# Performance work log

Measured on AMD Instinct MI355X. Metric: run time of the kernel, lower is better.

## Reference

```python
import jax, jax.numpy as jnp
import numpy as np

B, S, D = 2, 1024, 1024
H, KV, HD = 16, 4, 64
E, F = 8, 3584
EPS = 1e-5
TOP_K = 2


def setup_inputs() -> dict:
    key = jax.random.key(0)
    ks = jax.random.split(key, 12)
    sc = 0.02
    inv_freq = 1.0 / (10000.0 ** (np.arange(0, HD, 2, dtype=np.float32) / HD))
    freqs = np.outer(np.arange(S, dtype=np.float32), inv_freq)
    emb = np.concatenate([freqs, freqs], axis=-1)  # [S, HD]
    return {
        'x': jax.random.normal(ks[0], (B, S, D), jnp.float32),
        'ln1_w': jnp.ones((D,), jnp.float32),
        'ln2_w': jnp.ones((D,), jnp.float32),
        'wq': jax.random.normal(ks[1], (H * HD, D), jnp.float32) * sc,
        'wk': jax.random.normal(ks[2], (KV * HD, D), jnp.float32) * sc,
        'wv': jax.random.normal(ks[3], (KV * HD, D), jnp.float32) * sc,
        'wo': jax.random.normal(ks[4], (D, H * HD), jnp.float32) * sc,
        'gate_w': jax.random.normal(ks[5], (E, D), jnp.float32) * sc,
        'w1': jax.random.normal(ks[6], (E, F, D), jnp.float32) * sc,
        'w2': jax.random.normal(ks[7], (E, D, F), jnp.float32) * sc,
        'w3': jax.random.normal(ks[8], (E, F, D), jnp.float32) * sc,
        'cos': jnp.asarray(np.cos(emb)),
        'sin': jnp.asarray(np.sin(emb)),
    }


def _rms_norm(x, w):
    var = jnp.mean(jnp.square(x), axis=-1, keepdims=True)
    return x * jax.lax.rsqrt(var + EPS) * w


def _rotate_half(x):
    x1, x2 = jnp.split(x, 2, axis=-1)
    return jnp.concatenate([-x2, x1], axis=-1)


def _attn(h, wq, wk, wv, wo, cos, sin):
    # h: [B,S,D]
    q = (h @ wq.T).reshape(B, S, H, HD).transpose(0, 2, 1, 3)      # [B,H,S,HD]
    k = (h @ wk.T).reshape(B, S, KV, HD).transpose(0, 2, 1, 3)     # [B,KV,S,HD]
    v = (h @ wv.T).reshape(B, S, KV, HD).transpose(0, 2, 1, 3)
    c = cos[None, None, :S, :]
    s = sin[None, None, :S, :]
    q = q * c + _rotate_half(q) * s
    k = k * c + _rotate_half(k) * s
    k = jnp.repeat(k, H // KV, axis=1)  # GQA expand -> [B,H,S,HD]
    v = jnp.repeat(v, H // KV, axis=1)
    scores = jnp.einsum('bhqd,bhkd->bhqk', q, k) / jnp.sqrt(jnp.float32(HD))
    causal = jnp.tril(jnp.ones((S, S), bool))
    scores = jnp.where(causal[None, None], scores, jnp.float32(-1e30))
    probs = jax.nn.softmax(scores, axis=-1)
    out = jnp.einsum('bhqk,bhkd->bhqd', probs, v)
    out = out.transpose(0, 2, 1, 3).reshape(B, S, H * HD)
    return out @ wo.T


def _moe(h, gate_w, w1, w2, w3):
    T = B * S
    hs = h.reshape(T, D)
    probs = jax.nn.softmax(hs @ gate_w.T, axis=-1)       # [T,E]
    _, sel = jax.lax.top_k(probs, TOP_K)                  # [T,2]
    rw = jnp.take_along_axis(probs, sel, axis=-1)
    rw = rw / jnp.sum(rw, axis=-1, keepdims=True)
    cw = jnp.zeros((T, E), hs.dtype).at[jnp.arange(T)[:, None], sel].add(rw)  # [T,E] combine weights
    h1 = jnp.einsum('td,efd->tef', hs, w1)               # [T,E,F]
    h3 = jnp.einsum('td,efd->tef', hs, w3)
    inter = jax.nn.silu(h1) * h3
    out = jnp.einsum('tef,edf,te->td', inter, w2, cw)
    return out.reshape(B, S, D)


def reference(x, ln1_w, ln2_w, wq, wk, wv, wo, gate_w, w1, w2, w3, cos, sin):
    h = x + _attn(_rms_norm(x, ln1_w), wq, wk, wv, wo, cos, sin)
    h = h + _moe(_rms_norm(h, ln2_w), gate_w, w1, w2, w3)
    return h
```

## Files before the change

### kernel.cpp

```cpp
#include <hip/hip_runtime.h>

typedef unsigned short u16;
using short8 = __attribute__((ext_vector_type(8))) short;
using f32x4  = __attribute__((ext_vector_type(4))) float;

#define TQ   2048
#define DM   1024
#define SLEN 1024
#define FDIM 3584
#define NEXP 8

static __device__ __forceinline__ u16 f2bf(float f) {
  union { float f; unsigned u; } a; a.f = f;
  unsigned r = a.u + 0x7fffu + ((a.u >> 16) & 1u);
  return (u16)(r >> 16);
}
static __device__ __forceinline__ float bf2f(u16 u) {
  union { unsigned u; float f; } a; a.u = ((unsigned)u) << 16;
  return a.f;
}
static __device__ __forceinline__ unsigned cvtpk(float lo, float hi) {
  unsigned r;
  asm volatile("v_cvt_pk_bf16_f32 %0, %1, %2" : "=v"(r) : "v"(lo), "v"(hi));
  return r;
}

static __device__ __forceinline__ void gload16(const void* g, void* l) {
  __builtin_amdgcn_global_load_lds((const __attribute__((address_space(1))) void*)g,
                                   (__attribute__((address_space(3))) void*)l, 16, 0, 0);
}

static __device__ __forceinline__ int swz64(int bid) {
  return (bid & ~63) | ((bid & 7) << 3) | ((bid >> 3) & 7);
}

static __device__ __forceinline__ short8 ldW(const float* base, int row, int g) {
  const float* rp = base + row * 32;
  int x0 = (((g << 1) ^ (row & 7)) << 2);
  int x1 = ((((g << 1) | 1) ^ (row & 7)) << 2);
  float4 f0 = *(const float4*)(rp + x0);
  float4 f1 = *(const float4*)(rp + x1);
  union { uint4 u; short8 s; } c;
  c.u.x = cvtpk(f0.x, f0.y); c.u.y = cvtpk(f0.z, f0.w);
  c.u.z = cvtpk(f1.x, f1.y); c.u.w = cvtpk(f1.z, f1.w);
  return c.s;
}

__global__ __launch_bounds__(256) void rmsnorm_kernel(
    const float* __restrict__ x, const float* __restrict__ w,
    u16* __restrict__ oh, u16* __restrict__ ol, float* __restrict__ of) {
  int t = blockIdx.x, tid = threadIdx.x;
  const float4* xr = (const float4*)(x + (size_t)t * DM);
  float4 v = xr[tid];
  float ss = v.x * v.x + v.y * v.y + v.z * v.z + v.w * v.w;
#pragma unroll
  for (int m = 1; m < 64; m <<= 1) ss += __shfl_xor(ss, m);
  __shared__ float red[4];
  if ((tid & 63) == 0) red[tid >> 6] = ss;
  __syncthreads();
  float tot = red[0] + red[1] + red[2] + red[3];
  float sc = rsqrtf(tot * (1.0f / DM) + 1e-5f);
  float4 wv = ((const float4*)w)[tid];
  float o0 = v.x * sc * wv.x, o1 = v.y * sc * wv.y, o2 = v.z * sc * wv.z, o3 = v.w * sc * wv.w;
  ushort4 hh;
  hh.x = f2bf(o0); hh.y = f2bf(o1); hh.z = f2bf(o2); hh.w = f2bf(o3);
  *(ushort4*)(oh + (size_t)t * DM + tid * 4) = hh;
  if (ol) {
    ushort4 ll;
    ll.x = f2bf(o0 - bf2f(hh.x)); ll.y = f2bf(o1 - bf2f(hh.y));
    ll.z = f2bf(o2 - bf2f(hh.z)); ll.w = f2bf(o3 - bf2f(hh.w));
    *(ushort4*)(ol + (size_t)t * DM + tid * 4) = ll;
  }
  if (of) {
    float4 o4; o4.x = o0; o4.y = o1; o4.z = o2; o4.w = o3;
    ((float4*)(of + (size_t)t * DM))[tid] = o4;
  }
}

__global__ __launch_bounds__(256) void wconv_split_kernel(
    const float* __restrict__ wq, const float* __restrict__ wk,
    const float* __restrict__ wv, const float* __restrict__ wo,
    u16* __restrict__ qkvh, u16* __restrict__ qkvl,
    u16* __restrict__ woh, u16* __restrict__ wol) {
  for (int i = blockIdx.x * 256 + threadIdx.x; i < 655360; i += 640 * 256) {
    int el = i * 4;
    const float* src; u16 *dh, *dl;
    if (el < 1572864) {
      int r = el >> 10, c = el & 1023;
      if (r < 1024) src = wq + el;
      else if (r < 1280) src = wk + (r - 1024) * 1024 + c;
      else src = wv + (r - 1280) * 1024 + c;
      dh = qkvh + el; dl = qkvl + el;
    } else {
      int e2 = el - 1572864;
      src = wo + e2; dh = woh + e2; dl = wol + e2;
    }
    float4 v = *(const float4*)src;
    ushort4 h, l;
    h.x = f2bf(v.x); h.y = f2bf(v.y); h.z = f2bf(v.z); h.w = f2bf(v.w);
    l.x = f2bf(v.x - bf2f(h.x)); l.y = f2bf(v.y - bf2f(h.y));
    l.z = f2bf(v.z - bf2f(h.z)); l.w = f2bf(v.w - bf2f(h.w));
    *(ushort4*)dh = h; *(ushort4*)dl = l;
  }
}

template <bool RESID>
__global__ __launch_bounds__(256) void gemm_split2_kernel(
    const u16* __restrict__ Ah, const u16* __restrict__ Al,
    const u16* __restrict__ Wh, const u16* __restrict__ Wl,
    float* __restrict__ C, const float* __restrict__ resid, int N) {
  __shared__ u16 sAh[2][128][32], sAl[2][128][32], sWh[2][64][32], sWl[2][64][32];
  int lid = swz64(blockIdx.x);
  int bm = lid & 15, bn = lid >> 4;
  int tid = threadIdx.x, lane = tid & 63, w = tid >> 6;
  int wm = w >> 1, wn = w & 1;
  int qi = lane & 15, g = lane >> 4;
  int lr = lane >> 2, lc = (lane & 3) * 8;
  const u16* pa0 = Ah + (size_t)(bm * 128 + w * 16 + lr) * DM + lc;
  const u16* pa1 = pa0 + 64 * DM;
  const u16* pl0 = Al + (size_t)(bm * 128 + w * 16 + lr) * DM + lc;
  const u16* pl1 = pl0 + 64 * DM;
  const u16* pw  = Wh + (size_t)(bn * 64 + w * 16 + lr) * DM + lc;
  const u16* pwl = Wl + (size_t)(bn * 64 + w * 16 + lr) * DM + lc;
  f32x4 acc[4][2] = {};
#define STG2(buf, kk) do { \
    gload16(pa0 + (kk), &sAh[buf][w * 16][0]); \
    gload16(pa1 + (kk), &sAh[buf][64 + w * 16][0]); \
    gload16(pl0 + (kk), &sAl[buf][w * 16][0]); \
    gload16(pl1 + (kk), &sAl[buf][64 + w * 16][0]); \
    gload16(pw  + (kk), &sWh[buf][w * 16][0]); \
    gload16(pwl + (kk), &sWl[buf][w * 16][0]); } while (0)
  STG2(0, 0);
  asm volatile("s_waitcnt vmcnt(0)" ::: "memory");
  __syncthreads();
  for (int ks = 0; ks < 32; ks++) {
    int cur = ks & 1;
    if (ks < 31) STG2(cur ^ 1, (ks + 1) * 32);
    short8 afh[4], afl[4], bfh[2], bfl[2];
#pragma unroll
    for (int i = 0; i < 4; i++) {
      afh[i] = *(short8*)&sAh[cur][wm * 64 + i * 16 + qi][g * 8];
      afl[i] = *(short8*)&sAl[cur][wm * 64 + i * 16 + qi][g * 8];
    }
#pragma unroll
    for (int i = 0; i < 2; i++) {
      bfh[i] = *(short8*)&sWh[cur][wn * 32 + i * 16 + qi][g * 8];
      bfl[i] = *(short8*)&sWl[cur][wn * 32 + i * 16 + qi][g * 8];
    }
#pragma unroll
    for (int mi = 0; mi < 4; mi++)
#pragma unroll
      for (int ni = 0; ni < 2; ni++) {
        f32x4 a = acc[mi][ni];
        a = __builtin_amdgcn_mfma_f32_16x16x32_bf16(afh[mi], bfh[ni], a, 0, 0, 0);
        a = __builtin_amdgcn_mfma_f32_16x16x32_bf16(afl[mi], bfh[ni], a, 0, 0, 0);
        a = __builtin_amdgcn_mfma_f32_16x16x32_bf16(afh[mi], bfl[ni], a, 0, 0, 0);
        acc[mi][ni] = a;
      }
    asm volatile("s_waitcnt vmcnt(0)" ::: "memory");
    __syncthreads();
  }
#undef STG2
#pragma unroll
  for (int mi = 0; mi < 4; mi++)
#pragma unroll
    for (int ni = 0; ni < 2; ni++) {
      int col = bn * 64 + wn * 32 + ni * 16 + qi;
#pragma unroll
      for (int r = 0; r < 4; r++) {
        int row = bm * 128 + wm * 64 + mi * 16 + g * 4 + r;
        float val = acc[mi][ni][r];
        if (RESID) val += resid[(size_t)row * N + col];
        C[(size_t)row * N + col] = val;
      }
    }
}

__global__ __launch_bounds__(256) void rope_split_kernel(
    const float* __restrict__ qkvf,
    const float* __restrict__ cosT, const float* __restrict__ sinT,
    u16* __restrict__ qh, u16* __restrict__ ql, u16* __restrict__ kh, u16* __restrict__ kl,
    u16* __restrict__ vh, u16* __restrict__ vl) {
  int t = blockIdx.x, tid = threadIdx.x;
  int s = t & (SLEN - 1);
  const float* rowp = qkvf + (size_t)t * 1536;
#pragma unroll
  for (int it = 0; it < 2; it++) {
    int i = it * 256 + tid;
    int hh = i >> 5, d = i & 31;
    float c = cosT[s * 64 + d], sn = sinT[s * 64 + d];
    size_t dst = (size_t)t * DM + hh * 64 + d;
    float x1 = rowp[hh * 64 + d], x2 = rowp[hh * 64 + d + 32];
    float o1 = x1 * c - x2 * sn;
    float o2 = x2 * c + x1 * sn;
    u16 h1 = f2bf(o1), h2 = f2bf(o2);
    qh[dst] = h1; qh[dst + 32] = h2;
    ql[dst] = f2bf(o1 - bf2f(h1)); ql[dst + 32] = f2bf(o2 - bf2f(h2));
  }
  if (tid < 128) {
    int hh = tid >> 5, d = tid & 31;
    float c = cosT[s * 64 + d], sn = sinT[s * 64 + d];
    size_t dst = (size_t)t * 256 + hh * 64 + d;
    float x1 = rowp[1024 + hh * 64 + d], x2 = rowp[1024 + hh * 64 + d + 32];
    float o1 = x1 * c - x2 * sn;
    float o2 = x2 * c + x1 * sn;
    u16 h1 = f2bf(o1), h2 = f2bf(o2);
    kh[dst] = h1; kh[dst + 32] = h2;
    kl[dst] = f2bf(o1 - bf2f(h1)); kl[dst + 32] = f2bf(o2 - bf2f(h2));
  }
  {
    size_t dst = (size_t)t * 256 + tid;
    float v = rowp[1280 + tid];
    u16 h = f2bf(v);
    vh[dst] = h; vl[dst] = f2bf(v - bf2f(h));
  }
}

__global__ __launch_bounds__(256) void attn_kernel(
    const u16* __restrict__ qh, const u16* __restrict__ ql,
    const u16* __restrict__ kh, const u16* __restrict__ kl,
    const u16* __restrict__ vh, const u16* __restrict__ vl,
    u16* __restrict__ oh, u16* __restrict__ ol) {
  __shared__ u16 sKh[64][72], sKl[64][72];
  __shared__ u16 sVh[64][72], sVl[64][72];
  __shared__ u16 sPh[4][16][72], sPl[4][16][72];
  int qt = blockIdx.x & 15;
  int bh = blockIdx.x >> 4;
  int b = bh >> 4, h = bh & 15, kvh = h >> 2;
  int tid = threadIdx.x, lane = tid & 63, w = tid >> 6;
  int qi = lane & 15, g = lane >> 4;
  int qrow = qt * 64 + w * 16 + qi;
  size_t qbase = ((size_t)(b * SLEN + qrow)) * DM + h * 64;
  short8 qfh[2], qfl[2];
#pragma unroll
  for (int ds = 0; ds < 2; ds++) {
    qfh[ds] = *(const short8*)(qh + qbase + ds * 32 + g * 8);
    qfl[ds] = *(const short8*)(ql + qbase + ds * 32 + g * 8);
  }
  f32x4 oacc[4] = {};
  float mrun = -1e30f, lrun = 0.f;
  int ktiles = qt + 1;
  for (int kt = 0; kt < ktiles; kt++) {
    __syncthreads();
    {
      int r = tid >> 3, cs = (tid & 7) * 8;
#pragma unroll
      for (int rr = 0; rr < 64; rr += 32) {
        int key = kt * 64 + rr + r;
        size_t src = ((size_t)(b * SLEN + key)) * 256 + kvh * 64 + cs;
        *(short8*)&sKh[rr + r][cs] = *(const short8*)(kh + src);
        *(short8*)&sKl[rr + r][cs] = *(const short8*)(kl + src);
        short8 vv = *(const short8*)(vh + src);
        short8 vv2 = *(const short8*)(vl + src);
#pragma unroll
        for (int j = 0; j < 8; j++) {
          sVh[cs + j][rr + r] = (u16)vv[j];
          sVl[cs + j][rr + r] = (u16)vv2[j];
        }
      }
    }
    __syncthreads();
    f32x4 sa[4];
#pragma unroll
    for (int kf = 0; kf < 4; kf++) {
      f32x4 a = {};
#pragma unroll
      for (int ds = 0; ds < 2; ds++) {
        short8 kfh = *(short8*)&sKh[kf * 16 + qi][ds * 32 + g * 8];
        short8 kfl = *(short8*)&sKl[kf * 16 + qi][ds * 32 + g * 8];
        a = __builtin_amdgcn_mfma_f32_16x16x32_bf16(kfh, qfh[ds], a, 0, 0, 0);
        a = __builtin_amdgcn_mfma_f32_16x16x32_bf16(kfl, qfh[ds], a, 0, 0, 0);
        a = __builtin_amdgcn_mfma_f32_16x16x32_bf16(kfh, qfl[ds], a, 0, 0, 0);
      }
      sa[kf] = a;
    }
    int qg = qt * 64 + w * 16 + qi;
    float sv[4][4];
    float tmax = -1e30f;
#pragma unroll
    for (int kf = 0; kf < 4; kf++)
#pragma unroll
      for (int r = 0; r < 4; r++) {
        int key = kt * 64 + kf * 16 + g * 4 + r;
        float s = sa[kf][r] * 0.125f;
        s = (key <= qg) ? s : -1e30f;
        sv[kf][r] = s;
        tmax = fmaxf(tmax, s);
      }
    tmax = fmaxf(tmax, __shfl_xor(tmax, 16));
    tmax = fmaxf(tmax, __shfl_xor(tmax, 32));
    float mn = fmaxf(mrun, tmax);
    float alpha = expf(mrun - mn);
    float psum = 0.f;
#pragma unroll
    for (int kf = 0; kf < 4; kf++) {
      float p0 = expf(sv[kf][0] - mn), p1 = expf(sv[kf][1] - mn);
      float p2 = expf(sv[kf][2] - mn), p3 = expf(sv[kf][3] - mn);
      psum += p0 + p1 + p2 + p3;
      ushort4 ph, pl;
      ph.x = f2bf(p0); ph.y = f2bf(p1); ph.z = f2bf(p2); ph.w = f2bf(p3);
      pl.x = f2bf(p0 - bf2f(ph.x)); pl.y = f2bf(p1 - bf2f(ph.y));
      pl.z = f2bf(p2 - bf2f(ph.z)); pl.w = f2bf(p3 - bf2f(ph.w));
      *(ushort4*)&sPh[w][qi][kf * 16 + g * 4] = ph;
      *(ushort4*)&sPl[w][qi][kf * 16 + g * 4] = pl;
    }
    psum += __shfl_xor(psum, 16);
    psum += __shfl_xor(psum, 32);
    lrun = lrun * alpha + psum;
    mrun = mn;
#pragma unroll
    for (int df = 0; df < 4; df++) {
      oacc[df][0] *= alpha; oacc[df][1] *= alpha;
      oacc[df][2] *= alpha; oacc[df][3] *= alpha;
    }
#pragma unroll
    for (int ks = 0; ks < 2; ks++) {
      short8 pfh = *(short8*)&sPh[w][qi][ks * 32 + g * 8];
      short8 pfl = *(short8*)&sPl[w][qi][ks * 32 + g * 8];
#pragma unroll
      for (int df = 0; df < 4; df++) {
        short8 vfh = *(short8*)&sVh[df * 16 + qi][ks * 32 + g * 8];
        short8 vfl = *(short8*)&sVl[df * 16 + qi][ks * 32 + g * 8];
        f32x4 a = oacc[df];
        a = __builtin_amdgcn_mfma_f32_16x16x32_bf16(vfh, pfh, a, 0, 0, 0);
        a = __builtin_amdgcn_mfma_f32_16x16x32_bf16(vfl, pfh, a, 0, 0, 0);
        a = __builtin_amdgcn_mfma_f32_16x16x32_bf16(vfh, pfl, a, 0, 0, 0);
        oacc[df] = a;
      }
    }
  }
  float inv = 1.0f / lrun;
  size_t obase = ((size_t)(b * SLEN + qt * 64 + w * 16 + qi)) * DM + h * 64;
#pragma unroll
  for (int df = 0; df < 4; df++) {
    float o0 = oacc[df][0] * inv, o1 = oacc[df][1] * inv;
    float o2 = oacc[df][2] * inv, o3 = oacc[df][3] * inv;
    ushort4 hh, ll;
    hh.x = f2bf(o0); hh.y = f2bf(o1); hh.z = f2bf(o2); hh.w = f2bf(o3);
    ll.x = f2bf(o0 - bf2f(hh.x)); ll.y = f2bf(o1 - bf2f(hh.y));
    ll.z = f2bf(o2 - bf2f(hh.z)); ll.w = f2bf(o3 - bf2f(hh.w));
    *(ushort4*)(oh + obase + df * 16 + g * 4) = hh;
    *(ushort4*)(ol + obase + df * 16 + g * 4) = ll;
  }
}

__global__ void zero8_kernel(int* p) { if (threadIdx.x < 8) p[threadIdx.x] = 0; }

__global__ __launch_bounds__(64) void gate_kernel(
    const float* __restrict__ hf, const float* __restrict__ gw,
    int* cnt, int* tok_e, int* tok_pos, float* tok_w) {
  int t = blockIdx.x, lane = threadIdx.x;
  float acc[8] = {0, 0, 0, 0, 0, 0, 0, 0};
  for (int i = lane; i < DM; i += 64) {
    float h = hf[(size_t)t * DM + i];
#pragma unroll
    for (int e = 0; e < 8; e++) acc[e] += h * gw[e * DM + i];
  }
#pragma unroll
  for (int e = 0; e < 8; e++)
#pragma unroll
    for (int m = 1; m < 64; m <<= 1) acc[e] += __shfl_xor(acc[e], m);
  if (lane == 0) {
    int i0 = 0;
#pragma unroll
    for (int e = 1; e < 8; e++) if (acc[e] > acc[i0]) i0 = e;
    int i1 = -1;
#pragma unroll
    for (int e = 0; e < 8; e++) if (e != i0 && (i1 < 0 || acc[e] > acc[i1])) i1 = e;
    float w0 = 1.0f;
    float w1 = expf(acc[i1] - acc[i0]);
    float rs = 1.0f / (w0 + w1);
    int p0 = atomicAdd(&cnt[i0], 1);
    int p1 = atomicAdd(&cnt[i1], 1);
    tok_e[t * 2] = i0; tok_e[t * 2 + 1] = i1;
    tok_pos[t * 2] = p0; tok_pos[t * 2 + 1] = p1;
    tok_w[t * 2] = w0 * rs; tok_w[t * 2 + 1] = w1 * rs;
  }
}

__global__ void schedule_kernel(const int* cnt, int* offs, int* mt,
                                int* row_e, int* row_bm) {
  if (threadIdx.x == 0) {
    int s = 0, m = 0;
    for (int e = 0; e < 8; e++) {
      offs[e] = s;
      int nb = (cnt[e] + 127) >> 7;
      for (int i = 0; i < nb; i++) { row_e[m] = e; row_bm[m] = i; m++; }
      s += cnt[e];
    }
    *mt = m;
  }
}

__global__ __launch_bounds__(256) void gather_kernel(
    const u16* __restrict__ hn2b, const int* __restrict__ tok_e,
    const int* __restrict__ tok_pos, const float* __restrict__ tok_w,
    const int* __restrict__ offs, u16* __restrict__ Xg,
    int* __restrict__ pair_tok, int* __restrict__ pair_slot, float* __restrict__ pair_w) {
  int t = blockIdx.x;
#pragma unroll
  for (int slot = 0; slot < 2; slot++) {
    int e = tok_e[t * 2 + slot];
    int p = offs[e] + tok_pos[t * 2 + slot];
    ((ushort4*)(Xg + (size_t)p * DM))[threadIdx.x] =
        ((const ushort4*)(hn2b + (size_t)t * DM))[threadIdx.x];
    if (threadIdx.x == 0) {
      pair_tok[p] = t; pair_slot[p] = slot; pair_w[p] = tok_w[t * 2 + slot];
    }
  }
}

__global__ __launch_bounds__(256) void moe_gemm13_kernel(
    const u16* __restrict__ Xg, const float* __restrict__ w1,
    const float* __restrict__ w3, const int* __restrict__ cnt,
    const int* __restrict__ offs, const int* __restrict__ mt,
    const int* __restrict__ row_e, const int* __restrict__ row_bm,
    u16* __restrict__ inter) {
  __shared__ u16 sA[3][128][32];
  __shared__ float sW1[3][64][32], sW3[3][64][32];
  int lid = swz64(blockIdx.x);
  int MT = *mt;
  if (lid >= MT * 56) return;
  int mrow = lid % MT, bn = lid / MT;
  int e = row_e[mrow], bm = row_bm[mrow];
  int count = cnt[e], off = offs[e];
  const u16* A = Xg + (size_t)off * DM;
  const float* W1 = w1 + (size_t)e * FDIM * DM;
  const float* W3 = w3 + (size_t)e * FDIM * DM;
  int tid = threadIdx.x, lane = tid & 63, w = tid >> 6;
  int wm = w >> 1, wn = w & 1;
  int qi = lane & 15, g = lane >> 4;
  int lrA = lane >> 2, lcA = (lane & 3) * 8;
  int ga0 = bm * 128 + w * 32 + lrA;      if (ga0 >= count) ga0 = count - 1;
  int ga1 = bm * 128 + w * 32 + 16 + lrA; if (ga1 >= count) ga1 = count - 1;
  const u16* pa0 = A + (size_t)ga0 * DM + lcA;
  const u16* pa1 = A + (size_t)ga1 * DM + lcA;
  int usw = ((lane & 7) ^ (lane >> 3)) * 4;
  int rw0 = w * 16 + (lane >> 3);
  const float* p10 = W1 + (size_t)(bn * 64 + rw0) * DM + usw;
  const float* p11 = W1 + (size_t)(bn * 64 + rw0 + 8) * DM + usw;
  const float* p30 = W3 + (size_t)(bn * 64 + rw0) * DM + usw;
  const float* p31 = W3 + (size_t)(bn * 64 + rw0 + 8) * DM + usw;
  f32x4 acc1[4][2] = {}, acc3[4][2] = {};
#define STG13(buf, kk) do { \
    gload16(pa0 + (kk), &sA[buf][w * 32][0]); \
    gload16(pa1 + (kk), &sA[buf][w * 32 + 16][0]); \
    gload16(p10 + (kk), &sW1[buf][w * 16][0]); \
    gload16(p11 + (kk), &sW1[buf][w * 16 + 8][0]); \
    gload16(p30 + (kk), &sW3[buf][w * 16][0]); \
    gload16(p31 + (kk), &sW3[buf][w * 16 + 8][0]); } while (0)
  STG13(0, 0);
  STG13(1, 32);
  for (int ks = 0; ks < 32; ks++) {
    int cur = ks % 3;
    if (ks < 31) asm volatile("s_waitcnt vmcnt(6)" ::: "memory");
    else         asm volatile("s_waitcnt vmcnt(0)" ::: "memory");
    __builtin_amdgcn_s_barrier();
    short8 af[4];
#pragma unroll
    for (int i = 0; i < 4; i++)
      af[i] = *(short8*)&sA[cur][wm * 64 + i * 16 + qi][g * 8];
    short8 b1[2], b3[2];
#pragma unroll
    for (int ni = 0; ni < 2; ni++) {
      int rt = wn * 32 + ni * 16 + qi;
      b1[ni] = ldW(&sW1[cur][0][0], rt, g);
      b3[ni] = ldW(&sW3[cur][0][0], rt, g);
    }
#pragma unroll
    for (int mi = 0; mi < 4; mi++)
#pragma unroll
      for (int ni = 0; ni < 2; ni++) {
        acc1[mi][ni] = __builtin_amdgcn_mfma_f32_16x16x32_bf16(af[mi], b1[ni], acc1[mi][ni], 0, 0, 0);
        acc3[mi][ni] = __builtin_amdgcn_mfma_f32_16x16x32_bf16(af[mi], b3[ni], acc3[mi][ni], 0, 0, 0);
      }
    if (ks < 30) STG13((ks + 2) % 3, (ks + 2) * 32);
  }
#undef STG13
#pragma unroll
  for (int mi = 0; mi < 4; mi++)
#pragma unroll
    for (int r = 0; r < 4; r++) {
      int row = bm * 128 + wm * 64 + mi * 16 + g * 4 + r;
      if (row < count) {
        size_t obase = (size_t)(off + row) * FDIM + bn * 64 + wn * 32;
#pragma unroll
        for (int ni = 0; ni < 2; ni++) {
          float c1 = acc1[mi][ni][r], c3 = acc3[mi][ni][r];
          float sv = c1 / (1.0f + expf(-c1)) * c3;
          inter[obase + ni * 16 + qi] = f2bf(sv);
        }
      }
    }
}

__global__ __launch_bounds__(256) void moe_gemm2_kernel(
    const u16* __restrict__ inter, const float* __restrict__ w2,
    const int* __restrict__ cnt, const int* __restrict__ offs,
    const int* __restrict__ mt, const int* __restrict__ row_e,
    const int* __restrict__ row_bm,
    const int* __restrict__ pair_tok, const int* __restrict__ pair_slot,
    const float* __restrict__ pair_w, float* __restrict__ pout) {
  __shared__ u16 sA[3][128][32];
  __shared__ float sW[3][128][32];
  int lid = swz64(blockIdx.x);
  int MT = *mt;
  if (lid >= MT * 8) return;
  int mrow = lid % MT, bn = lid / MT;
  int e = row_e[mrow], bm = row_bm[mrow];
  int count = cnt[e], off = offs[e];
  const u16* A = inter + (size_t)off * FDIM;
  const float* W = w2 + (size_t)e * DM * FDIM;
  int tid = threadIdx.x, lane = tid & 63, w = tid >> 6;
  int wm = w >> 1, wn = w & 1;
  int qi = lane & 15, g = lane >> 4;
  int lrA = lane >> 2, lcA = (lane & 3) * 8;
  int ga0 = bm * 128 + w * 32 + lrA;      if (ga0 >= count) ga0 = count - 1;
  int ga1 = bm * 128 + w * 32 + 16 + lrA; if (ga1 >= count) ga1 = count - 1;
  const u16* pa0 = A + (size_t)ga0 * FDIM + lcA;
  const u16* pa1 = A + (size_t)ga1 * FDIM + lcA;
  int usw = ((lane & 7) ^ (lane >> 3)) * 4;
  int rwb = w * 32 + (lane >> 3);
  const float* pw0 = W + (size_t)(bn * 128 + rwb) * FDIM + usw;
  const float* pw1 = W + (size_t)(bn * 128 + rwb + 8) * FDIM + usw;
  const float* pw2 = W + (size_t)(bn * 128 + rwb + 16) * FDIM + usw;
  const float* pw3 = W + (size_t)(bn * 128 + rwb + 24) * FDIM + usw;
  f32x4 acc[4][4] = {};
#define STG2M(buf, kk) do { \
    gload16(pa0 + (kk), &sA[buf][w * 32][0]); \
    gload16(pa1 + (kk), &sA[buf][w * 32 + 16][0]); \
    gload16(pw0 + (kk), &sW[buf][w * 32][0]); \
    gload16(pw1 + (kk), &sW[buf][w * 32 + 8][0]); \
    gload16(pw2 + (kk), &sW[buf][w * 32 + 16][0]); \
    gload16(pw3 + (kk), &sW[buf][w * 32 + 24][0]); } while (0)
  STG2M(0, 0);
  STG2M(1, 32);
  const int NK = FDIM / 32;
  for (int ks = 0; ks < NK; ks++) {
    int cur = ks % 3;
    if (ks < NK - 1) asm volatile("s_waitcnt vmcnt(6)" ::: "memory");
    else             asm volatile("s_waitcnt vmcnt(0)" ::: "memory");
    __builtin_amdgcn_s_barrier();
    short8 af[4];
#pragma unroll
    for (int i = 0; i < 4; i++)
      af[i] = *(short8*)&sA[cur][wm * 64 + i * 16 + qi][g * 8];
    short8 bfr[4];
#pragma unroll
    for (int ni = 0; ni < 4; ni++) {
      int rt = wn * 64 + ni * 16 + qi;
      bfr[ni] = ldW(&sW[cur][0][0], rt, g);
    }
#pragma unroll
    for (int mi = 0; mi < 4; mi++)
#pragma unroll
      for (int ni = 0; ni < 4; ni++)
        acc[mi][ni] = __builtin_amdgcn_mfma_f32_16x16x32_bf16(af[mi], bfr[ni], acc[mi][ni], 0, 0, 0);
    if (ks < NK - 2) STG2M((ks + 2) % 3, (ks + 2) * 32);
  }
#undef STG2M
#pragma unroll
  for (int mi = 0; mi < 4; mi++)
#pragma unroll
    for (int r = 0; r < 4; r++) {
      int row = bm * 128 + wm * 64 + mi * 16 + g * 4 + r;
      if (row < count) {
        int p = off + row;
        int t = pair_tok[p];
        float wgt = pair_w[p];
        size_t obase = ((size_t)pair_slot[p] * TQ + t) * DM + bn * 128 + wn * 64;
#pragma unroll
        for (int ni = 0; ni < 4; ni++)
          pout[obase + ni * 16 + qi] = acc[mi][ni][r] * wgt;
      }
    }
}

__global__ __launch_bounds__(256) void combine_kernel(
    const float* __restrict__ h, const float* __restrict__ pout, float* __restrict__ out) {
  size_t i = (size_t)blockIdx.x * 256 + threadIdx.x;
  float4 a = ((const float4*)h)[i];
  float4 b0 = ((const float4*)pout)[i];
  float4 b1 = ((const float4*)pout)[i + (size_t)TQ * DM / 4];
  float4 r;
  r.x = a.x + b0.x + b1.x; r.y = a.y + b0.y + b1.y;
  r.z = a.z + b0.z + b1.z; r.w = a.w + b0.w + b1.w;
  ((float4*)out)[i] = r;
}

extern "C" void kernel_launch(void* const* d_in, const int* in_sizes, int n_in,
                              void* d_out, int out_size, void* d_ws, size_t ws_size,
                              hipStream_t stream) {
  (void)in_sizes; (void)n_in; (void)out_size; (void)ws_size;
  const float* x    = (const float*)d_in[0];
  const float* ln1  = (const float*)d_in[1];
  const float* ln2  = (const float*)d_in[2];
  const float* wq   = (const float*)d_in[3];
  const float* wk   = (const float*)d_in[4];
  const float* wv   = (const float*)d_in[5];
  const float* wo   = (const float*)d_in[6];
  const float* gw   = (const float*)d_in[7];
  const float* w1   = (const float*)d_in[8];
  const float* w2   = (const float*)d_in[9];
  const float* w3   = (const float*)d_in[10];
  const float* cosT = (const float*)d_in[11];
  const float* sinT = (const float*)d_in[12];

  char* mb = (char*)d_ws;
  const size_t MB = 1024 * 1024;
  u16*   qhb  = (u16*)(mb + 0 * MB);
  u16*   qlb  = (u16*)(mb + 4 * MB);
  u16*   khb  = (u16*)(mb + 8 * MB);
  u16*   klb  = (u16*)(mb + 9 * MB);
  u16*   vhb  = (u16*)(mb + 10 * MB);
  u16*   vlb  = (u16*)(mb + 11 * MB);
  u16*   hn2b = (u16*)(mb + 0 * MB);
  float* hn2f = (float*)(mb + 4 * MB);
  u16*   ahb  = (u16*)(mb + 12 * MB);
  u16*   alb  = (u16*)(mb + 16 * MB);
  u16*   Xg   = (u16*)(mb + 12 * MB);
  u16*   hn1h = (u16*)(mb + 20 * MB);
  u16*   hn1l = (u16*)(mb + 24 * MB);
  u16*   inter= (u16*)(mb + 20 * MB);
  float* qkvf = (float*)(mb + 28 * MB);
  float* h_res= (float*)(mb + 48 * MB);
  u16*   woh  = (u16*)(mb + 56 * MB);
  u16*   wol  = (u16*)(mb + 58 * MB);
  float* pout = (float*)(mb + 56 * MB);
  u16*   wqkvh= (u16*)(mb + 60 * MB);
  u16*   wqkvl= (u16*)(mb + 63 * MB);
  int*   cnt  = (int*)(mb + 72 * MB);
  int*   offs = cnt + 8;
  int*   mtp  = cnt + 16;
  int*   row_e  = cnt + 17;
  int*   row_bm = cnt + 57;
  int*   tok_e  = cnt + 128;
  int*   tok_pos = tok_e + 4096;
  float* tok_w   = (float*)(tok_pos + 4096);
  int*   pair_tok  = (int*)(tok_w + 4096);
  int*   pair_slot = pair_tok + 4096;
  float* pair_w    = (float*)(pair_slot + 4096);

  wconv_split_kernel<<<640, 256, 0, stream>>>(wq, wk, wv, wo, wqkvh, wqkvl, woh, wol);
  rmsnorm_kernel<<<TQ, 256, 0, stream>>>(x, ln1, hn1h, hn1l, nullptr);
  gemm_split2_kernel<false><<<384, 256, 0, stream>>>(hn1h, hn1l, wqkvh, wqkvl, qkvf, nullptr, 1536);
  rope_split_kernel<<<TQ, 256, 0, stream>>>(qkvf, cosT, sinT, qhb, qlb, khb, klb, vhb, vlb);
  attn_kernel<<<512, 256, 0, stream>>>(qhb, qlb, khb, klb, vhb, vlb, ahb, alb);
  gemm_split2_kernel<true><<<256, 256, 0, stream>>>(ahb, alb, woh, wol, h_res, x, 1024);
  rmsnorm_kernel<<<TQ, 256, 0, stream>>>(h_res, ln2, hn2b, nullptr, hn2f);
  zero8_kernel<<<1, 64, 0, stream>>>(cnt);
  gate_kernel<<<TQ, 64, 0, stream>>>(hn2f, gw, cnt, tok_e, tok_pos, tok_w);
  schedule_kernel<<<1, 64, 0, stream>>>(cnt, offs, mtp, row_e, row_bm);
  gather_kernel<<<TQ, 256, 0, stream>>>(hn2b, tok_e, tok_pos, tok_w, offs, Xg,
                                        pair_tok, pair_slot, pair_w);
  moe_gemm13_kernel<<<2240, 256, 0, stream>>>(Xg, w1, w3, cnt, offs, mtp,
                                              row_e, row_bm, inter);
  moe_gemm2_kernel<<<320, 256, 0, stream>>>(inter, w2, cnt, offs, mtp,
                                            row_e, row_bm,
                                            pair_tok, pair_slot, pair_w, pout);
  combine_kernel<<<TQ, 256, 0, stream>>>(h_res, pout, (float*)d_out);
}
```

Baseline: 501.7 us.

## Stage MoE expert weights through registers, storing bf16 in LDS

In both MoE GEMM kernels, the fp32 expert weights no longer go straight into LDS via global_load_lds. They are loaded into registers, converted to bf16 once per element and written into a swizzled bf16 LDS tile, one stage ahead of use. This halves the LDS footprint and read traffic for weights and removes the repeated fp32-to-bf16 conversion each wave did on every LDS read. In exchange it adds register pressure and hand-tuned vmcnt/lgkmcnt waits that must match the new mix of register loads and async LDS loads.

```diff
diff --git a/kernel.cpp b/kernel.cpp
--- a/kernel.cpp
+++ b/kernel.cpp
@@ -34,16 +34,11 @@
   return (bid & ~63) | ((bid & 7) << 3) | ((bid >> 3) & 7);
 }
 
-static __device__ __forceinline__ short8 ldW(const float* base, int row, int g) {
-  const float* rp = base + row * 32;
-  int x0 = (((g << 1) ^ (row & 7)) << 2);
-  int x1 = ((((g << 1) | 1) ^ (row & 7)) << 2);
-  float4 f0 = *(const float4*)(rp + x0);
-  float4 f1 = *(const float4*)(rp + x1);
-  union { uint4 u; short8 s; } c;
-  c.u.x = cvtpk(f0.x, f0.y); c.u.y = cvtpk(f0.z, f0.w);
-  c.u.z = cvtpk(f1.x, f1.y); c.u.w = cvtpk(f1.z, f1.w);
-  return c.s;
+static __device__ __forceinline__ void cvtwr8(float4 a, float4 b, u16* dst) {
+  uint4 u;
+  u.x = cvtpk(a.x, a.y); u.y = cvtpk(a.z, a.w);
+  u.z = cvtpk(b.x, b.y); u.w = cvtpk(b.z, b.w);
+  *(uint4*)dst = u;
 }
 
 __global__ __launch_bounds__(256) void rmsnorm_kernel(
@@ -417,7 +412,7 @@
     const int* __restrict__ row_e, const int* __restrict__ row_bm,
     u16* __restrict__ inter) {
   __shared__ u16 sA[3][128][32];
-  __shared__ float sW1[3][64][32], sW3[3][64][32];
+  __shared__ u16 sW1[3][64][32], sW3[3][64][32];
   int lid = swz64(blockIdx.x);
   int MT = *mt;
   if (lid >= MT * 56) return;
@@ -435,37 +430,41 @@
   int ga1 = bm * 128 + w * 32 + 16 + lrA; if (ga1 >= count) ga1 = count - 1;
   const u16* pa0 = A + (size_t)ga0 * DM + lcA;
   const u16* pa1 = A + (size_t)ga1 * DM + lcA;
-  int usw = ((lane & 7) ^ (lane >> 3)) * 4;
-  int rw0 = w * 16 + (lane >> 3);
-  const float* p10 = W1 + (size_t)(bn * 64 + rw0) * DM + usw;
-  const float* p11 = W1 + (size_t)(bn * 64 + rw0 + 8) * DM + usw;
-  const float* p30 = W3 + (size_t)(bn * 64 + rw0) * DM + usw;
-  const float* p31 = W3 + (size_t)(bn * 64 + rw0 + 8) * DM + usw;
+  int r16 = lane >> 2;
+  int rW = w * 16 + r16;
+  int cW = (lane & 3) * 8;
+  const float* q1 = W1 + (size_t)(bn * 64 + rW) * DM + cW;
+  const float* q3 = W3 + (size_t)(bn * 64 + rW) * DM + cW;
+  int uW = ((lane & 3) ^ (r16 & 3)) * 8;
   f32x4 acc1[4][2] = {}, acc3[4][2] = {};
-#define STG13(buf, kk) do { \
-    gload16(pa0 + (kk), &sA[buf][w * 32][0]); \
-    gload16(pa1 + (kk), &sA[buf][w * 32 + 16][0]); \
-    gload16(p10 + (kk), &sW1[buf][w * 16][0]); \
-    gload16(p11 + (kk), &sW1[buf][w * 16 + 8][0]); \
-    gload16(p30 + (kk), &sW3[buf][w * 16][0]); \
-    gload16(p31 + (kk), &sW3[buf][w * 16 + 8][0]); } while (0)
-  STG13(0, 0);
-  STG13(1, 32);
+  float4 p1a = *(const float4*)q1, p1b = *(const float4*)(q1 + 4);
+  float4 p3a = *(const float4*)q3, p3b = *(const float4*)(q3 + 4);
+  float4 v1a = *(const float4*)(q1 + 32), v1b = *(const float4*)(q1 + 36);
+  float4 v3a = *(const float4*)(q3 + 32), v3b = *(const float4*)(q3 + 36);
+  __builtin_amdgcn_sched_barrier(0);
+  gload16(pa0, &sA[0][w * 32][0]);
+  gload16(pa1, &sA[0][w * 32 + 16][0]);
+  gload16(pa0 + 32, &sA[1][w * 32][0]);
+  gload16(pa1 + 32, &sA[1][w * 32 + 16][0]);
+  asm volatile("s_waitcnt vmcnt(8)" ::: "memory");
+  cvtwr8(p1a, p1b, &sW1[0][rW][uW]);
+  cvtwr8(p3a, p3b, &sW3[0][rW][uW]);
   for (int ks = 0; ks < 32; ks++) {
     int cur = ks % 3;
-    if (ks < 31) asm volatile("s_waitcnt vmcnt(6)" ::: "memory");
-    else         asm volatile("s_waitcnt vmcnt(0)" ::: "memory");
+    if (ks == 0)       asm volatile("s_waitcnt vmcnt(2) lgkmcnt(0)" ::: "memory");
+    else if (ks == 31) asm volatile("s_waitcnt vmcnt(0) lgkmcnt(0)" ::: "memory");
+    else               asm volatile("s_waitcnt vmcnt(6) lgkmcnt(0)" ::: "memory");
     __builtin_amdgcn_s_barrier();
-    short8 af[4];
+    short8 af[4], b1[2], b3[2];
 #pragma unroll
     for (int i = 0; i < 4; i++)
       af[i] = *(short8*)&sA[cur][wm * 64 + i * 16 + qi][g * 8];
-    short8 b1[2], b3[2];
 #pragma unroll
     for (int ni = 0; ni < 2; ni++) {
       int rt = wn * 32 + ni * 16 + qi;
-      b1[ni] = ldW(&sW1[cur][0][0], rt, g);
-      b3[ni] = ldW(&sW3[cur][0][0], rt, g);
+      int ui = (g ^ (rt & 3)) * 8;
+      b1[ni] = *(short8*)&sW1[cur][rt][ui];
+      b3[ni] = *(short8*)&sW3[cur][rt][ui];
     }
 #pragma unroll
     for (int mi = 0; mi < 4; mi++)
@@ -474,9 +473,21 @@
         acc1[mi][ni] = __builtin_amdgcn_mfma_f32_16x16x32_bf16(af[mi], b1[ni], acc1[mi][ni], 0, 0, 0);
         acc3[mi][ni] = __builtin_amdgcn_mfma_f32_16x16x32_bf16(af[mi], b3[ni], acc3[mi][ni], 0, 0, 0);
       }
-    if (ks < 30) STG13((ks + 2) % 3, (ks + 2) * 32);
-  }
-#undef STG13
+    if (ks < 31) {
+      int nb = (ks + 1) % 3;
+      cvtwr8(v1a, v1b, &sW1[nb][rW][uW]);
+      cvtwr8(v3a, v3b, &sW3[nb][rW][uW]);
+      if (ks < 30) {
+        int k2 = (ks + 2) * 32;
+        v1a = *(const float4*)(q1 + k2); v1b = *(const float4*)(q1 + k2 + 4);
+        v3a = *(const float4*)(q3 + k2); v3b = *(const float4*)(q3 + k2 + 4);
+        __builtin_amdgcn_sched_barrier(0);
+        int ab = (ks + 2) % 3;
+        gload16(pa0 + k2, &sA[ab][w * 32][0]);
+        gload16(pa1 + k2, &sA[ab][w * 32 + 16][0]);
+      }
+    }
+  }
 #pragma unroll
   for (int mi = 0; mi < 4; mi++)
 #pragma unroll
@@ -502,7 +513,7 @@
     const int* __restrict__ pair_tok, const int* __restrict__ pair_slot,
     const float* __restrict__ pair_w, float* __restrict__ pout) {
   __shared__ u16 sA[3][128][32];
-  __shared__ float sW[3][128][32];
+  __shared__ u16 sW[3][128][32];
   int lid = swz64(blockIdx.x);
   int MT = *mt;
   if (lid >= MT * 8) return;
@@ -519,46 +530,62 @@
   int ga1 = bm * 128 + w * 32 + 16 + lrA; if (ga1 >= count) ga1 = count - 1;
   const u16* pa0 = A + (size_t)ga0 * FDIM + lcA;
   const u16* pa1 = A + (size_t)ga1 * FDIM + lcA;
-  int usw = ((lane & 7) ^ (lane >> 3)) * 4;
-  int rwb = w * 32 + (lane >> 3);
-  const float* pw0 = W + (size_t)(bn * 128 + rwb) * FDIM + usw;
-  const float* pw1 = W + (size_t)(bn * 128 + rwb + 8) * FDIM + usw;
-  const float* pw2 = W + (size_t)(bn * 128 + rwb + 16) * FDIM + usw;
-  const float* pw3 = W + (size_t)(bn * 128 + rwb + 24) * FDIM + usw;
+  int r32 = lane >> 1;
+  int rW = w * 32 + r32;
+  int cW = (lane & 1) * 16;
+  const float* qw = W + (size_t)(bn * 128 + rW) * FDIM + cW;
+  int ug = (lane & 1) * 2;
+  int u0 = (ug ^ (r32 & 3)) * 8;
+  int u1 = ((ug | 1) ^ (r32 & 3)) * 8;
   f32x4 acc[4][4] = {};
-#define STG2M(buf, kk) do { \
-    gload16(pa0 + (kk), &sA[buf][w * 32][0]); \
-    gload16(pa1 + (kk), &sA[buf][w * 32 + 16][0]); \
-    gload16(pw0 + (kk), &sW[buf][w * 32][0]); \
-    gload16(pw1 + (kk), &sW[buf][w * 32 + 8][0]); \
-    gload16(pw2 + (kk), &sW[buf][w * 32 + 16][0]); \
-    gload16(pw3 + (kk), &sW[buf][w * 32 + 24][0]); } while (0)
-  STG2M(0, 0);
-  STG2M(1, 32);
+  float4 pa_ = *(const float4*)qw,        pb_ = *(const float4*)(qw + 4);
+  float4 pc_ = *(const float4*)(qw + 8),  pd_ = *(const float4*)(qw + 12);
+  float4 va = *(const float4*)(qw + 32),  vb = *(const float4*)(qw + 36);
+  float4 vc = *(const float4*)(qw + 40),  vd = *(const float4*)(qw + 44);
+  __builtin_amdgcn_sched_barrier(0);
+  gload16(pa0, &sA[0][w * 32][0]);
+  gload16(pa1, &sA[0][w * 32 + 16][0]);
+  gload16(pa0 + 32, &sA[1][w * 32][0]);
+  gload16(pa1 + 32, &sA[1][w * 32 + 16][0]);
+  asm volatile("s_waitcnt vmcnt(8)" ::: "memory");
+  cvtwr8(pa_, pb_, &sW[0][rW][u0]);
+  cvtwr8(pc_, pd_, &sW[0][rW][u1]);
   const int NK = FDIM / 32;
   for (int ks = 0; ks < NK; ks++) {
     int cur = ks % 3;
-    if (ks < NK - 1) asm volatile("s_waitcnt vmcnt(6)" ::: "memory");
-    else             asm volatile("s_waitcnt vmcnt(0)" ::: "memory");
+    if (ks == 0)           asm volatile("s_waitcnt vmcnt(2) lgkmcnt(0)" ::: "memory");
+    else if (ks == NK - 1) asm volatile("s_waitcnt vmcnt(0) lgkmcnt(0)" ::: "memory");
+    else                   asm volatile("s_waitcnt vmcnt(6) lgkmcnt(0)" ::: "memory");
     __builtin_amdgcn_s_barrier();
-    short8 af[4];
+    short8 af[4], bfr[4];
 #pragma unroll
     for (int i = 0; i < 4; i++)
       af[i] = *(short8*)&sA[cur][wm * 64 + i * 16 + qi][g * 8];
-    short8 bfr[4];
 #pragma unroll
     for (int ni = 0; ni < 4; ni++) {
       int rt = wn * 64 + ni * 16 + qi;
-      bfr[ni] = ldW(&sW[cur][0][0], rt, g);
+      bfr[ni] = *(short8*)&sW[cur][rt][(g ^ (rt & 3)) * 8];
     }
 #pragma unroll
     for (int mi = 0; mi < 4; mi++)
 #pragma unroll
       for (int ni = 0; ni < 4; ni++)
         acc[mi][ni] = __builtin_amdgcn_mfma_f32_16x16x32_bf16(af[mi], bfr[ni], acc[mi][ni], 0, 0, 0);
-    if (ks < NK - 2) STG2M((ks + 2) % 3, (ks + 2) * 32);
-  }
-#undef STG2M
+    if (ks < NK - 1) {
+      int nb = (ks + 1) % 3;
+      cvtwr8(va, vb, &sW[nb][rW][u0]);
+      cvtwr8(vc, vd, &sW[nb][rW][u1]);
+      if (ks < NK - 2) {
+        int k2 = (ks + 2) * 32;
+        va = *(const float4*)(qw + k2);      vb = *(const float4*)(qw + k2 + 4);
+        vc = *(const float4*)(qw + k2 + 8);  vd = *(const float4*)(qw + k2 + 12);
+        __builtin_amdgcn_sched_barrier(0);
+        int ab = (ks + 2) % 3;
+        gload16(pa0 + k2, &sA[ab][w * 32][0]);
+        gload16(pa1 + k2, &sA[ab][w * 32 + 16][0]);
+      }
+    }
+  }
 #pragma unroll
   for (int mi = 0; mi < 4; mi++)
 #pragma unroll
```

Result: no change. 510.2 us (+1.7%).
